# Kernel optimization log

Measured on AMD Instinct MI355X. Metric: run time of the kernel, lower is better.

## Reference

```python
import jax, jax.numpy as jnp
import numpy as np

HEADS = 8
EMBED = 512


def setup_inputs() -> dict:
    key = jax.random.key(0)
    ks = jax.random.split(key, 9)
    N, KL, QL, S = 4, 512, 32, 64
    D = EMBED // HEADS
    return {
        "values": jax.random.normal(ks[0], (N, KL, EMBED), jnp.float32),
        "keys": jax.random.normal(ks[1], (N, KL, EMBED), jnp.float32),
        "query": jax.random.normal(ks[2], (N, QL, S, EMBED), jnp.float32),
        "mask": jax.random.randint(ks[3], (N, 1, 1, KL, 1), 0, 2, jnp.int32),
        "Wv": jax.random.normal(ks[4], (D, D), jnp.float32) * 0.05,
        "Wk": jax.random.normal(ks[5], (D, D), jnp.float32) * 0.05,
        "Wq": jax.random.normal(ks[6], (D, D), jnp.float32) * 0.05,
        "Wo": jax.random.normal(ks[7], (EMBED, EMBED), jnp.float32) * 0.05,
        "bo": jax.random.normal(ks[8], (EMBED,), jnp.float32) * 0.05,
    }


def reference(values, keys, query, mask, Wv, Wk, Wq, Wo, bo):
    N, KL, E = keys.shape
    QL, S = query.shape[1], query.shape[2]
    H = HEADS
    D = E // H
    # split heads, then per-head linear (weights shared across heads, torch y = x @ W.T)
    v = jnp.einsum('nkhd,ed->nkhe', values.reshape(N, KL, H, D), Wv)
    k = jnp.einsum('nkhd,ed->nkhe', keys.reshape(N, KL, H, D), Wk)
    q = jnp.einsum('nqshd,ed->nqshe', query.reshape(N, QL, S, H, D), Wq)
    # energy: [N, H, QL, KL, S]
    energy = jnp.einsum('nqshd,nkhd->nhqks', q, k)
    energy = jnp.where(mask == 0, jnp.float32(-1e20), energy)
    scale = jnp.float32(E ** 0.5)
    attention = jax.nn.softmax(energy / scale, axis=3)  # softmax over key axis
    out = jnp.einsum('nhqks,nkhd->nqshd', attention, v).reshape(N, QL, S, E)
    return out @ Wo.T + bo
```

## Files before the change

kernel.cpp:

```cpp
#include <hip/hip_runtime.h>
#include <math.h>


typedef __bf16 bf16;
typedef __attribute__((ext_vector_type(8))) __bf16 bf16x8;
typedef __attribute__((ext_vector_type(4))) __bf16 bf16x4;
typedef __attribute__((ext_vector_type(4))) float f32x4;

#define LW 68
#define LS 72
#define QSCALE (0.044194173824159216f * 1.4426950408889634f)
#define MASK_BIAS -64.0f

__device__ __forceinline__ bf16x8 cvt8(const float* p, float s) {
    float4 x0 = *(const float4*)p;
    float4 x1 = *(const float4*)(p + 4);
    return (bf16x8){(bf16)(x0.x * s), (bf16)(x0.y * s), (bf16)(x0.z * s), (bf16)(x0.w * s),
                    (bf16)(x1.x * s), (bf16)(x1.y * s), (bf16)(x1.z * s), (bf16)(x1.w * s)};
}

__global__ __launch_bounds__(256, 2) void kv_proj(const float* __restrict__ keys,
                                                  const float* __restrict__ values,
                                                  const float* __restrict__ Wk,
                                                  const float* __restrict__ Wv,
                                                  bf16* __restrict__ Kp,
                                                  bf16* __restrict__ Vt) {
    __shared__ bf16 Xk[64 * LW];
    __shared__ bf16 Xv[64 * LW];
    int t = threadIdx.x;
    int nh = blockIdx.x >> 3, kt = blockIdx.x & 7;
    int n = nh >> 3, h = nh & 7, kl0 = kt * 64;
    int w = t >> 6, quad = (t >> 4) & 3, c16 = t & 15;
#pragma unroll
    for (int i = 0; i < 4; ++i) {
        int f = t + i * 256, row = f >> 4, c4 = f & 15;
        float4 a = *(const float4*)(keys + ((long)n * 512 + kl0 + row) * 512 + h * 64 + c4 * 4);
        float4 b = *(const float4*)(values + ((long)n * 512 + kl0 + row) * 512 + h * 64 + c4 * 4);
        *(bf16x4*)&Xk[row * LW + c4 * 4] = (bf16x4){(bf16)a.x, (bf16)a.y, (bf16)a.z, (bf16)a.w};
        *(bf16x4*)&Xv[row * LW + c4 * 4] = (bf16x4){(bf16)b.x, (bf16)b.y, (bf16)b.z, (bf16)b.w};
    }
    __syncthreads();
    if (w < 2) {
        bf16x8 wf[8];
#pragma unroll
        for (int nb = 0; nb < 4; ++nb)
#pragma unroll
            for (int kc = 0; kc < 2; ++kc)
                wf[nb * 2 + kc] = cvt8(Wk + (16 * nb + c16) * 64 + 32 * kc + quad * 8, 1.0f);
        f32x4 acc[2][4];
#pragma unroll
        for (int mb = 0; mb < 2; ++mb)
#pragma unroll
            for (int nb = 0; nb < 4; ++nb) acc[mb][nb] = (f32x4){0.f, 0.f, 0.f, 0.f};
#pragma unroll
        for (int kc = 0; kc < 2; ++kc) {
            bf16x8 a0 = *(const bf16x8*)&Xk[(32 * w + c16) * LW + 32 * kc + quad * 8];
            bf16x8 a1 = *(const bf16x8*)&Xk[(32 * w + 16 + c16) * LW + 32 * kc + quad * 8];
#pragma unroll
            for (int nb = 0; nb < 4; ++nb) {
                acc[0][nb] = __builtin_amdgcn_mfma_f32_16x16x32_bf16(a0, wf[nb * 2 + kc], acc[0][nb], 0, 0, 0);
                acc[1][nb] = __builtin_amdgcn_mfma_f32_16x16x32_bf16(a1, wf[nb * 2 + kc], acc[1][nb], 0, 0, 0);
            }
        }
#pragma unroll
        for (int mb = 0; mb < 2; ++mb)
#pragma unroll
            for (int nb = 0; nb < 4; ++nb)
#pragma unroll
                for (int r = 0; r < 4; ++r)
                    Kp[((long)nh * 512 + kl0 + 32 * w + 16 * mb + quad * 4 + r) * 64 + 16 * nb + c16] =
                        (bf16)acc[mb][nb][r];
    } else {
        int w2 = w - 2;
        bf16x8 af[4];
#pragma unroll
        for (int mb = 0; mb < 2; ++mb)
#pragma unroll
            for (int kc = 0; kc < 2; ++kc)
                af[mb * 2 + kc] = cvt8(Wv + (32 * w2 + 16 * mb + c16) * 64 + 32 * kc + quad * 8, 1.0f);
        f32x4 acc[2][4];
#pragma unroll
        for (int mb = 0; mb < 2; ++mb)
#pragma unroll
            for (int nb = 0; nb < 4; ++nb) acc[mb][nb] = (f32x4){0.f, 0.f, 0.f, 0.f};
#pragma unroll
        for (int kc = 0; kc < 2; ++kc) {
#pragma unroll
            for (int nb = 0; nb < 4; ++nb) {
                bf16x8 b = *(const bf16x8*)&Xv[(16 * nb + c16) * LW + 32 * kc + quad * 8];
                acc[0][nb] = __builtin_amdgcn_mfma_f32_16x16x32_bf16(af[kc], b, acc[0][nb], 0, 0, 0);
                acc[1][nb] = __builtin_amdgcn_mfma_f32_16x16x32_bf16(af[2 + kc], b, acc[1][nb], 0, 0, 0);
            }
        }
#pragma unroll
        for (int mb = 0; mb < 2; ++mb)
#pragma unroll
            for (int nb = 0; nb < 4; ++nb)
#pragma unroll
                for (int r = 0; r < 4; ++r)
                    Vt[((long)nh * 64 + 32 * w2 + 16 * mb + quad * 4 + r) * 512 + kl0 + 16 * nb + c16] =
                        (bf16)acc[mb][nb][r];
    }
}

__global__ __launch_bounds__(256, 4) void attn(const float* __restrict__ query,
                                               const float* __restrict__ Wq,
                                               const bf16* __restrict__ Kp,
                                               const bf16* __restrict__ Vtg,
                                               const int* __restrict__ maskp,
                                               bf16* __restrict__ AO) {
    __shared__ bf16 SX[64 * LS];
    __shared__ bf16 Kt[64 * LW];
    __shared__ bf16 Vs[64 * LW];
    __shared__ float Mb[64];
    int t = threadIdx.x;
    int nh = blockIdx.x & 31, qtile = blockIdx.x >> 5;
    int n = nh >> 3, h = nh & 7;
    int r0 = qtile * 64;
    int w = t >> 6, quad = (t >> 4) & 3, c16 = t & 15;
    const bf16* Kb = Kp + (long)nh * 512 * 64;
    const bf16* Vb = Vtg + (long)nh * 64 * 512;

    int prow0 = t >> 3, pcol0 = t & 7;
    int prow1 = (t + 256) >> 3, pcol1 = t & 7;
    bf16x8 pk0 = *(const bf16x8*)(Kb + (long)prow0 * 64 + pcol0 * 8);
    bf16x8 pk1 = *(const bf16x8*)(Kb + (long)prow1 * 64 + pcol1 * 8);
    bf16x8 pv0 = *(const bf16x8*)(Vb + (long)prow0 * 512 + pcol0 * 8);
    bf16x8 pv1 = *(const bf16x8*)(Vb + (long)prow1 * 512 + pcol1 * 8);
    float mnext = 0.f;
    if (t < 64) mnext = maskp[n * 512 + t] ? 0.f : MASK_BIAS;

    bf16x8 wf[8];
#pragma unroll
    for (int nb = 0; nb < 4; ++nb)
#pragma unroll
        for (int kc = 0; kc < 2; ++kc)
            wf[nb * 2 + kc] = cvt8(Wq + (16 * nb + c16) * 64 + 32 * kc + quad * 8, QSCALE);

    {
        int l = t & 63;
        int rloc = 16 * w + (l >> 2);
        const float* qrow = query + ((long)n * 2048 + r0 + rloc) * 512 + h * 64;
#pragma unroll
        for (int j = 0; j < 4; ++j) {
            int c = (l & 3) + 4 * j;
            float4 a = *(const float4*)(qrow + c * 4);
            *(bf16x4*)&SX[rloc * LS + c * 4] = (bf16x4){(bf16)a.x, (bf16)a.y, (bf16)a.z, (bf16)a.w};
        }
    }
    f32x4 qa[4];
#pragma unroll
    for (int nb = 0; nb < 4; ++nb) qa[nb] = (f32x4){0.f, 0.f, 0.f, 0.f};
#pragma unroll
    for (int kc = 0; kc < 2; ++kc) {
        bf16x8 a = *(const bf16x8*)&SX[(16 * w + c16) * LS + 32 * kc + quad * 8];
#pragma unroll
        for (int nb = 0; nb < 4; ++nb)
            qa[nb] = __builtin_amdgcn_mfma_f32_16x16x32_bf16(a, wf[nb * 2 + kc], qa[nb], 0, 0, 0);
    }
#pragma unroll
    for (int nb = 0; nb < 4; ++nb)
#pragma unroll
        for (int r = 0; r < 4; ++r)
            SX[(16 * w + quad * 4 + r) * LS + 16 * nb + c16] = (bf16)qa[nb][r];
    bf16x8 qf[2];
#pragma unroll
    for (int kc = 0; kc < 2; ++kc)
        qf[kc] = *(const bf16x8*)&SX[(16 * w + c16) * LS + 32 * kc + quad * 8];

    f32x4 oacc[4];
#pragma unroll
    for (int mb = 0; mb < 4; ++mb) oacc[mb] = (f32x4){0.f, 0.f, 0.f, 0.f};
    float ps = 0.f;

    for (int kt = 0; kt < 8; ++kt) {
        if (kt) __syncthreads();
        *(bf16x8*)&Kt[prow0 * LW + pcol0 * 8] = pk0;
        *(bf16x8*)&Kt[prow1 * LW + pcol1 * 8] = pk1;
        *(bf16x8*)&Vs[prow0 * LW + pcol0 * 8] = pv0;
        *(bf16x8*)&Vs[prow1 * LW + pcol1 * 8] = pv1;
        if (t < 64) Mb[t] = mnext;
        __syncthreads();
        if (kt < 7) {
            const bf16* Kn = Kb + (long)(kt + 1) * 64 * 64;
            const bf16* Vn = Vb + (kt + 1) * 64;
            pk0 = *(const bf16x8*)(Kn + (long)prow0 * 64 + pcol0 * 8);
            pk1 = *(const bf16x8*)(Kn + (long)prow1 * 64 + pcol1 * 8);
            pv0 = *(const bf16x8*)(Vn + (long)prow0 * 512 + pcol0 * 8);
            pv1 = *(const bf16x8*)(Vn + (long)prow1 * 512 + pcol1 * 8);
            if (t < 64) mnext = maskp[n * 512 + (kt + 1) * 64 + t] ? 0.f : MASK_BIAS;
        }
        f32x4 sc[4];
#pragma unroll
        for (int mb = 0; mb < 4; ++mb) sc[mb] = *(const f32x4*)&Mb[16 * mb + quad * 4];
#pragma unroll
        for (int kc = 0; kc < 2; ++kc) {
#pragma unroll
            for (int mb = 0; mb < 4; ++mb) {
                bf16x8 ka = *(const bf16x8*)&Kt[(16 * mb + c16) * LW + 32 * kc + quad * 8];
                sc[mb] = __builtin_amdgcn_mfma_f32_16x16x32_bf16(ka, qf[kc], sc[mb], 0, 0, 0);
            }
        }
#pragma unroll
        for (int mb = 0; mb < 4; ++mb) {
            float p0 = exp2f(sc[mb][0]);
            float p1 = exp2f(sc[mb][1]);
            float p2 = exp2f(sc[mb][2]);
            float p3 = exp2f(sc[mb][3]);
            ps += (p0 + p1) + (p2 + p3);
            *(bf16x4*)&SX[(16 * w + c16) * LS + 16 * mb + quad * 4] =
                (bf16x4){(bf16)p0, (bf16)p1, (bf16)p2, (bf16)p3};
        }
#pragma unroll
        for (int kc = 0; kc < 2; ++kc) {
            bf16x8 pb = *(const bf16x8*)&SX[(16 * w + c16) * LS + 32 * kc + quad * 8];
#pragma unroll
            for (int mb = 0; mb < 4; ++mb) {
                bf16x8 va = *(const bf16x8*)&Vs[(16 * mb + c16) * LW + 32 * kc + quad * 8];
                oacc[mb] = __builtin_amdgcn_mfma_f32_16x16x32_bf16(va, pb, oacc[mb], 0, 0, 0);
            }
        }
    }
    ps += __shfl_xor(ps, 16);
    ps += __shfl_xor(ps, 32);
    float il = 1.0f / ps;
    int row_g = r0 + 16 * w + c16;
#pragma unroll
    for (int mb = 0; mb < 4; ++mb)
        *(bf16x4*)(AO + ((long)n * 2048 + row_g) * 512 + h * 64 + 16 * mb + quad * 4) =
            (bf16x4){(bf16)(oacc[mb][0] * il), (bf16)(oacc[mb][1] * il),
                     (bf16)(oacc[mb][2] * il), (bf16)(oacc[mb][3] * il)};
}

__global__ __launch_bounds__(256, 2) void out_gemm(const bf16* __restrict__ A,
                                                   const float* __restrict__ Wo,
                                                   const float* __restrict__ bo,
                                                   float* __restrict__ C) {
    __shared__ bf16 At[128 * LW];
    __shared__ bf16 Bt[64 * LW];
    int t = threadIdx.x;
    int br = blockIdx.x & 63, bc = blockIdx.x >> 6;
    int r0 = br * 128, c0 = bc * 64;
    int w = t >> 6, quad = (t >> 4) & 3, c16 = t & 15;
    int arow[4], acol[4], wrow[4], wcol[4];
#pragma unroll
    for (int i = 0; i < 4; ++i) {
        int f = t + i * 256;
        arow[i] = f >> 3;
        acol[i] = f & 7;
        wrow[i] = f >> 4;
        wcol[i] = f & 15;
    }
    bf16x8 pa[4];
    float4 pw[4];
#pragma unroll
    for (int i = 0; i < 4; ++i) {
        pa[i] = *(const bf16x8*)(A + (long)(r0 + arow[i]) * 512 + acol[i] * 8);
        pw[i] = *(const float4*)(Wo + (long)(c0 + wrow[i]) * 512 + wcol[i] * 4);
    }
    f32x4 acc[2][4];
#pragma unroll
    for (int mb = 0; mb < 2; ++mb)
#pragma unroll
        for (int nb = 0; nb < 4; ++nb) acc[mb][nb] = (f32x4){0.f, 0.f, 0.f, 0.f};
    for (int k0 = 0; k0 < 512; k0 += 64) {
        if (k0) __syncthreads();
#pragma unroll
        for (int i = 0; i < 4; ++i) {
            *(bf16x8*)&At[arow[i] * LW + acol[i] * 8] = pa[i];
            *(bf16x4*)&Bt[wrow[i] * LW + wcol[i] * 4] =
                (bf16x4){(bf16)pw[i].x, (bf16)pw[i].y, (bf16)pw[i].z, (bf16)pw[i].w};
        }
        __syncthreads();
        if (k0 < 448) {
#pragma unroll
            for (int i = 0; i < 4; ++i) {
                pa[i] = *(const bf16x8*)(A + (long)(r0 + arow[i]) * 512 + k0 + 64 + acol[i] * 8);
                pw[i] = *(const float4*)(Wo + (long)(c0 + wrow[i]) * 512 + k0 + 64 + wcol[i] * 4);
            }
        }
#pragma unroll
        for (int kc = 0; kc < 2; ++kc) {
            bf16x8 a0 = *(const bf16x8*)&At[(32 * w + c16) * LW + 32 * kc + quad * 8];
            bf16x8 a1 = *(const bf16x8*)&At[(32 * w + 16 + c16) * LW + 32 * kc + quad * 8];
#pragma unroll
            for (int nb = 0; nb < 4; ++nb) {
                bf16x8 b = *(const bf16x8*)&Bt[(16 * nb + c16) * LW + 32 * kc + quad * 8];
                acc[0][nb] = __builtin_amdgcn_mfma_f32_16x16x32_bf16(a0, b, acc[0][nb], 0, 0, 0);
                acc[1][nb] = __builtin_amdgcn_mfma_f32_16x16x32_bf16(a1, b, acc[1][nb], 0, 0, 0);
            }
        }
    }
#pragma unroll
    for (int mb = 0; mb < 2; ++mb)
#pragma unroll
        for (int nb = 0; nb < 4; ++nb) {
            float bias = bo[c0 + 16 * nb + c16];
#pragma unroll
            for (int r = 0; r < 4; ++r)
                C[(long)(r0 + 32 * w + 16 * mb + quad * 4 + r) * 512 + c0 + 16 * nb + c16] =
                    acc[mb][nb][r] + bias;
        }
}

extern "C" void kernel_launch(void* const* d_in, const int* in_sizes, int n_in,
                              void* d_out, int out_size, void* d_ws, size_t ws_size,
                              hipStream_t stream) {
    const float* values = (const float*)d_in[0];
    const float* keys   = (const float*)d_in[1];
    const float* query  = (const float*)d_in[2];
    const int*   maskp  = (const int*)d_in[3];
    const float* Wv     = (const float*)d_in[4];
    const float* Wk     = (const float*)d_in[5];
    const float* Wq     = (const float*)d_in[6];
    const float* Wo     = (const float*)d_in[7];
    const float* bo     = (const float*)d_in[8];
    float* out = (float*)d_out;

    bf16* ws = (bf16*)d_ws;
    bf16* Kp = ws;
    bf16* Vt = Kp + 1048576;
    bf16* AO = Vt + 1048576;

    kv_proj<<<dim3(256), dim3(256), 0, stream>>>(keys, values, Wk, Wv, Kp, Vt);
    attn<<<dim3(1024), dim3(256), 0, stream>>>(query, Wq, Kp, Vt, maskp, AO);
    out_gemm<<<dim3(512), dim3(256), 0, stream>>>(AO, Wo, bo, out);
}
```

Before: 129.0 us.

## Split attention over key halves and merge partials in output GEMM

The attention kernel splits the key range into two halves per query tile, doubling the grid. Each half writes unnormalized bf16 partial outputs and row sums, and the output GEMM sums the two partials and normalizes while loading its A tile. The KV projection and output GEMM tiles are shrunk to launch more blocks, and the mask is read directly from global memory instead of staged in shared memory. This trades extra Q projection work and doubled intermediate traffic for higher occupancy and parallelism.

```diff
diff --git a/kernel.cpp b/kernel.cpp
--- a/kernel.cpp
+++ b/kernel.cpp
@@ -25,14 +25,14 @@
                                                   const float* __restrict__ Wv,
                                                   bf16* __restrict__ Kp,
                                                   bf16* __restrict__ Vt) {
-    __shared__ bf16 Xk[64 * LW];
-    __shared__ bf16 Xv[64 * LW];
+    __shared__ bf16 Xk[32 * LW];
+    __shared__ bf16 Xv[32 * LW];
     int t = threadIdx.x;
-    int nh = blockIdx.x >> 3, kt = blockIdx.x & 7;
-    int n = nh >> 3, h = nh & 7, kl0 = kt * 64;
+    int nh = blockIdx.x >> 4, klt = blockIdx.x & 15;
+    int n = nh >> 3, h = nh & 7, kl0 = klt * 32;
     int w = t >> 6, quad = (t >> 4) & 3, c16 = t & 15;
 #pragma unroll
-    for (int i = 0; i < 4; ++i) {
+    for (int i = 0; i < 2; ++i) {
         int f = t + i * 256, row = f >> 4, c4 = f & 15;
         float4 a = *(const float4*)(keys + ((long)n * 512 + kl0 + row) * 512 + h * 64 + c4 * 4);
         float4 b = *(const float4*)(values + ((long)n * 512 + kl0 + row) * 512 + h * 64 + c4 * 4);
@@ -41,61 +41,47 @@
     }
     __syncthreads();
     if (w < 2) {
-        bf16x8 wf[8];
+        f32x4 acc[4];
+#pragma unroll
+        for (int nb = 0; nb < 4; ++nb) acc[nb] = (f32x4){0.f, 0.f, 0.f, 0.f};
+#pragma unroll
+        for (int kc = 0; kc < 2; ++kc) {
+            bf16x8 a = *(const bf16x8*)&Xk[(16 * w + c16) * LW + 32 * kc + quad * 8];
+#pragma unroll
+            for (int nb = 0; nb < 4; ++nb) {
+                bf16x8 b = cvt8(Wk + (16 * nb + c16) * 64 + 32 * kc + quad * 8, 1.0f);
+                acc[nb] = __builtin_amdgcn_mfma_f32_16x16x32_bf16(a, b, acc[nb], 0, 0, 0);
+            }
+        }
 #pragma unroll
         for (int nb = 0; nb < 4; ++nb)
 #pragma unroll
-            for (int kc = 0; kc < 2; ++kc)
-                wf[nb * 2 + kc] = cvt8(Wk + (16 * nb + c16) * 64 + 32 * kc + quad * 8, 1.0f);
-        f32x4 acc[2][4];
-#pragma unroll
-        for (int mb = 0; mb < 2; ++mb)
-#pragma unroll
-            for (int nb = 0; nb < 4; ++nb) acc[mb][nb] = (f32x4){0.f, 0.f, 0.f, 0.f};
-#pragma unroll
-        for (int kc = 0; kc < 2; ++kc) {
-            bf16x8 a0 = *(const bf16x8*)&Xk[(32 * w + c16) * LW + 32 * kc + quad * 8];
-            bf16x8 a1 = *(const bf16x8*)&Xk[(32 * w + 16 + c16) * LW + 32 * kc + quad * 8];
-#pragma unroll
-            for (int nb = 0; nb < 4; ++nb) {
-                acc[0][nb] = __builtin_amdgcn_mfma_f32_16x16x32_bf16(a0, wf[nb * 2 + kc], acc[0][nb], 0, 0, 0);
-                acc[1][nb] = __builtin_amdgcn_mfma_f32_16x16x32_bf16(a1, wf[nb * 2 + kc], acc[1][nb], 0, 0, 0);
-            }
-        }
-#pragma unroll
-        for (int mb = 0; mb < 2; ++mb)
-#pragma unroll
-            for (int nb = 0; nb < 4; ++nb)
-#pragma unroll
-                for (int r = 0; r < 4; ++r)
-                    Kp[((long)nh * 512 + kl0 + 32 * w + 16 * mb + quad * 4 + r) * 64 + 16 * nb + c16] =
-                        (bf16)acc[mb][nb][r];
+            for (int r = 0; r < 4; ++r)
+                Kp[((long)nh * 512 + kl0 + 16 * w + quad * 4 + r) * 64 + 16 * nb + c16] =
+                    (bf16)acc[nb][r];
     } else {
         int w2 = w - 2;
-        bf16x8 af[4];
+        f32x4 acc[2][2];
 #pragma unroll
         for (int mb = 0; mb < 2; ++mb)
 #pragma unroll
-            for (int kc = 0; kc < 2; ++kc)
-                af[mb * 2 + kc] = cvt8(Wv + (32 * w2 + 16 * mb + c16) * 64 + 32 * kc + quad * 8, 1.0f);
-        f32x4 acc[2][4];
+            for (int nb = 0; nb < 2; ++nb) acc[mb][nb] = (f32x4){0.f, 0.f, 0.f, 0.f};
+#pragma unroll
+        for (int kc = 0; kc < 2; ++kc) {
+#pragma unroll
+            for (int mb = 0; mb < 2; ++mb) {
+                bf16x8 a = cvt8(Wv + (32 * w2 + 16 * mb + c16) * 64 + 32 * kc + quad * 8, 1.0f);
+#pragma unroll
+                for (int nb = 0; nb < 2; ++nb) {
+                    bf16x8 b = *(const bf16x8*)&Xv[(16 * nb + c16) * LW + 32 * kc + quad * 8];
+                    acc[mb][nb] = __builtin_amdgcn_mfma_f32_16x16x32_bf16(a, b, acc[mb][nb], 0, 0, 0);
+                }
+            }
+        }
 #pragma unroll
         for (int mb = 0; mb < 2; ++mb)
 #pragma unroll
-            for (int nb = 0; nb < 4; ++nb) acc[mb][nb] = (f32x4){0.f, 0.f, 0.f, 0.f};
-#pragma unroll
-        for (int kc = 0; kc < 2; ++kc) {
-#pragma unroll
-            for (int nb = 0; nb < 4; ++nb) {
-                bf16x8 b = *(const bf16x8*)&Xv[(16 * nb + c16) * LW + 32 * kc + quad * 8];
-                acc[0][nb] = __builtin_amdgcn_mfma_f32_16x16x32_bf16(af[kc], b, acc[0][nb], 0, 0, 0);
-                acc[1][nb] = __builtin_amdgcn_mfma_f32_16x16x32_bf16(af[2 + kc], b, acc[1][nb], 0, 0, 0);
-            }
-        }
-#pragma unroll
-        for (int mb = 0; mb < 2; ++mb)
-#pragma unroll
-            for (int nb = 0; nb < 4; ++nb)
+            for (int nb = 0; nb < 2; ++nb)
 #pragma unroll
                 for (int r = 0; r < 4; ++r)
                     Vt[((long)nh * 64 + 32 * w2 + 16 * mb + quad * 4 + r) * 512 + kl0 + 16 * nb + c16] =
@@ -108,27 +94,26 @@
                                                const bf16* __restrict__ Kp,
                                                const bf16* __restrict__ Vtg,
                                                const int* __restrict__ maskp,
-                                               bf16* __restrict__ AO) {
+                                               bf16* __restrict__ AOp,
+                                               float* __restrict__ Lb) {
     __shared__ bf16 SX[64 * LS];
     __shared__ bf16 Kt[64 * LW];
     __shared__ bf16 Vs[64 * LW];
-    __shared__ float Mb[64];
     int t = threadIdx.x;
-    int nh = blockIdx.x & 31, qtile = blockIdx.x >> 5;
+    int nh = blockIdx.x & 31, half = (blockIdx.x >> 5) & 1, qtile = blockIdx.x >> 6;
     int n = nh >> 3, h = nh & 7;
     int r0 = qtile * 64;
+    int kt0 = half * 4;
     int w = t >> 6, quad = (t >> 4) & 3, c16 = t & 15;
     const bf16* Kb = Kp + (long)nh * 512 * 64;
     const bf16* Vb = Vtg + (long)nh * 64 * 512;
 
     int prow0 = t >> 3, pcol0 = t & 7;
     int prow1 = (t + 256) >> 3, pcol1 = t & 7;
-    bf16x8 pk0 = *(const bf16x8*)(Kb + (long)prow0 * 64 + pcol0 * 8);
-    bf16x8 pk1 = *(const bf16x8*)(Kb + (long)prow1 * 64 + pcol1 * 8);
-    bf16x8 pv0 = *(const bf16x8*)(Vb + (long)prow0 * 512 + pcol0 * 8);
-    bf16x8 pv1 = *(const bf16x8*)(Vb + (long)prow1 * 512 + pcol1 * 8);
-    float mnext = 0.f;
-    if (t < 64) mnext = maskp[n * 512 + t] ? 0.f : MASK_BIAS;
+    bf16x8 pk0 = *(const bf16x8*)(Kb + (long)(kt0 * 64 + prow0) * 64 + pcol0 * 8);
+    bf16x8 pk1 = *(const bf16x8*)(Kb + (long)(kt0 * 64 + prow1) * 64 + pcol1 * 8);
+    bf16x8 pv0 = *(const bf16x8*)(Vb + (long)prow0 * 512 + kt0 * 64 + pcol0 * 8);
+    bf16x8 pv1 = *(const bf16x8*)(Vb + (long)prow1 * 512 + kt0 * 64 + pcol1 * 8);
 
     bf16x8 wf[8];
 #pragma unroll
@@ -173,26 +158,27 @@
     for (int mb = 0; mb < 4; ++mb) oacc[mb] = (f32x4){0.f, 0.f, 0.f, 0.f};
     float ps = 0.f;
 
-    for (int kt = 0; kt < 8; ++kt) {
+    for (int kt = 0; kt < 4; ++kt) {
+        int tk = kt0 + kt;
         if (kt) __syncthreads();
         *(bf16x8*)&Kt[prow0 * LW + pcol0 * 8] = pk0;
         *(bf16x8*)&Kt[prow1 * LW + pcol1 * 8] = pk1;
         *(bf16x8*)&Vs[prow0 * LW + pcol0 * 8] = pv0;
         *(bf16x8*)&Vs[prow1 * LW + pcol1 * 8] = pv1;
-        if (t < 64) Mb[t] = mnext;
         __syncthreads();
-        if (kt < 7) {
-            const bf16* Kn = Kb + (long)(kt + 1) * 64 * 64;
-            const bf16* Vn = Vb + (kt + 1) * 64;
-            pk0 = *(const bf16x8*)(Kn + (long)prow0 * 64 + pcol0 * 8);
-            pk1 = *(const bf16x8*)(Kn + (long)prow1 * 64 + pcol1 * 8);
-            pv0 = *(const bf16x8*)(Vn + (long)prow0 * 512 + pcol0 * 8);
-            pv1 = *(const bf16x8*)(Vn + (long)prow1 * 512 + pcol1 * 8);
-            if (t < 64) mnext = maskp[n * 512 + (kt + 1) * 64 + t] ? 0.f : MASK_BIAS;
+        if (kt < 3) {
+            pk0 = *(const bf16x8*)(Kb + (long)((tk + 1) * 64 + prow0) * 64 + pcol0 * 8);
+            pk1 = *(const bf16x8*)(Kb + (long)((tk + 1) * 64 + prow1) * 64 + pcol1 * 8);
+            pv0 = *(const bf16x8*)(Vb + (long)prow0 * 512 + (tk + 1) * 64 + pcol0 * 8);
+            pv1 = *(const bf16x8*)(Vb + (long)prow1 * 512 + (tk + 1) * 64 + pcol1 * 8);
         }
         f32x4 sc[4];
 #pragma unroll
-        for (int mb = 0; mb < 4; ++mb) sc[mb] = *(const f32x4*)&Mb[16 * mb + quad * 4];
+        for (int mb = 0; mb < 4; ++mb) {
+            int4 mk = *(const int4*)(maskp + n * 512 + tk * 64 + 16 * mb + quad * 4);
+            sc[mb] = (f32x4){mk.x ? 0.f : MASK_BIAS, mk.y ? 0.f : MASK_BIAS,
+                             mk.z ? 0.f : MASK_BIAS, mk.w ? 0.f : MASK_BIAS};
+        }
 #pragma unroll
         for (int kc = 0; kc < 2; ++kc) {
 #pragma unroll
@@ -223,84 +209,99 @@
     }
     ps += __shfl_xor(ps, 16);
     ps += __shfl_xor(ps, 32);
-    float il = 1.0f / ps;
     int row_g = r0 + 16 * w + c16;
+    bf16* AO = AOp + (long)half * 4194304;
 #pragma unroll
     for (int mb = 0; mb < 4; ++mb)
         *(bf16x4*)(AO + ((long)n * 2048 + row_g) * 512 + h * 64 + 16 * mb + quad * 4) =
-            (bf16x4){(bf16)(oacc[mb][0] * il), (bf16)(oacc[mb][1] * il),
-                     (bf16)(oacc[mb][2] * il), (bf16)(oacc[mb][3] * il)};
-}
-
-__global__ __launch_bounds__(256, 2) void out_gemm(const bf16* __restrict__ A,
+            (bf16x4){(bf16)oacc[mb][0], (bf16)oacc[mb][1], (bf16)oacc[mb][2], (bf16)oacc[mb][3]};
+    if (quad == 0) Lb[half * 65536 + nh * 2048 + row_g] = ps;
+}
+
+__global__ __launch_bounds__(256, 4) void out_gemm(const bf16* __restrict__ AOp,
+                                                   const float* __restrict__ Lb,
                                                    const float* __restrict__ Wo,
                                                    const float* __restrict__ bo,
                                                    float* __restrict__ C) {
-    __shared__ bf16 At[128 * LW];
+    __shared__ bf16 At[64 * LW];
     __shared__ bf16 Bt[64 * LW];
     int t = threadIdx.x;
-    int br = blockIdx.x & 63, bc = blockIdx.x >> 6;
-    int r0 = br * 128, c0 = bc * 64;
+    int br = blockIdx.x & 127, bc = blockIdx.x >> 7;
+    int r0 = br * 64, c0 = bc * 64;
     int w = t >> 6, quad = (t >> 4) & 3, c16 = t & 15;
-    int arow[4], acol[4], wrow[4], wcol[4];
-#pragma unroll
-    for (int i = 0; i < 4; ++i) {
+    const bf16* AO2 = AOp + 4194304;
+    int arow[2], acol[2], wrow[4], wcol[4];
+#pragma unroll
+    for (int i = 0; i < 2; ++i) {
         int f = t + i * 256;
         arow[i] = f >> 3;
         acol[i] = f & 7;
+    }
+#pragma unroll
+    for (int i = 0; i < 4; ++i) {
+        int f = t + i * 256;
         wrow[i] = f >> 4;
         wcol[i] = f & 15;
     }
-    bf16x8 pa[4];
+    bf16x8 pa1[2], pa2[2];
     float4 pw[4];
 #pragma unroll
-    for (int i = 0; i < 4; ++i) {
-        pa[i] = *(const bf16x8*)(A + (long)(r0 + arow[i]) * 512 + acol[i] * 8);
+    for (int i = 0; i < 2; ++i) {
+        pa1[i] = *(const bf16x8*)(AOp + (long)(r0 + arow[i]) * 512 + acol[i] * 8);
+        pa2[i] = *(const bf16x8*)(AO2 + (long)(r0 + arow[i]) * 512 + acol[i] * 8);
+    }
+#pragma unroll
+    for (int i = 0; i < 4; ++i)
         pw[i] = *(const float4*)(Wo + (long)(c0 + wrow[i]) * 512 + wcol[i] * 4);
-    }
-    f32x4 acc[2][4];
-#pragma unroll
-    for (int mb = 0; mb < 2; ++mb)
-#pragma unroll
-        for (int nb = 0; nb < 4; ++nb) acc[mb][nb] = (f32x4){0.f, 0.f, 0.f, 0.f};
+    f32x4 acc[4];
+#pragma unroll
+    for (int nb = 0; nb < 4; ++nb) acc[nb] = (f32x4){0.f, 0.f, 0.f, 0.f};
     for (int k0 = 0; k0 < 512; k0 += 64) {
+        int hh = k0 >> 6;
         if (k0) __syncthreads();
 #pragma unroll
-        for (int i = 0; i < 4; ++i) {
-            *(bf16x8*)&At[arow[i] * LW + acol[i] * 8] = pa[i];
+        for (int i = 0; i < 2; ++i) {
+            int grow = r0 + arow[i];
+            int lidx = ((grow >> 11) * 8 + hh) * 2048 + (grow & 2047);
+            float il = 1.0f / (Lb[lidx] + Lb[65536 + lidx]);
+            bf16x8 o;
+#pragma unroll
+            for (int e = 0; e < 8; ++e)
+                o[e] = (bf16)(((float)pa1[i][e] + (float)pa2[i][e]) * il);
+            *(bf16x8*)&At[arow[i] * LW + acol[i] * 8] = o;
+        }
+#pragma unroll
+        for (int i = 0; i < 4; ++i)
             *(bf16x4*)&Bt[wrow[i] * LW + wcol[i] * 4] =
                 (bf16x4){(bf16)pw[i].x, (bf16)pw[i].y, (bf16)pw[i].z, (bf16)pw[i].w};
-        }
         __syncthreads();
         if (k0 < 448) {
 #pragma unroll
-            for (int i = 0; i < 4; ++i) {
-                pa[i] = *(const bf16x8*)(A + (long)(r0 + arow[i]) * 512 + k0 + 64 + acol[i] * 8);
+            for (int i = 0; i < 2; ++i) {
+                pa1[i] = *(const bf16x8*)(AOp + (long)(r0 + arow[i]) * 512 + k0 + 64 + acol[i] * 8);
+                pa2[i] = *(const bf16x8*)(AO2 + (long)(r0 + arow[i]) * 512 + k0 + 64 + acol[i] * 8);
+            }
+#pragma unroll
+            for (int i = 0; i < 4; ++i)
                 pw[i] = *(const float4*)(Wo + (long)(c0 + wrow[i]) * 512 + k0 + 64 + wcol[i] * 4);
-            }
-        }
-#pragma unroll
-        for (int kc = 0; kc < 2; ++kc) {
-            bf16x8 a0 = *(const bf16x8*)&At[(32 * w + c16) * LW + 32 * kc + quad * 8];
-            bf16x8 a1 = *(const bf16x8*)&At[(32 * w + 16 + c16) * LW + 32 * kc + quad * 8];
+        }
+#pragma unroll
+        for (int kc = 0; kc < 2; ++kc) {
+            bf16x8 a = *(const bf16x8*)&At[(16 * w + c16) * LW + 32 * kc + quad * 8];
 #pragma unroll
             for (int nb = 0; nb < 4; ++nb) {
                 bf16x8 b = *(const bf16x8*)&Bt[(16 * nb + c16) * LW + 32 * kc + quad * 8];
-                acc[0][nb] = __builtin_amdgcn_mfma_f32_16x16x32_bf16(a0, b, acc[0][nb], 0, 0, 0);
-                acc[1][nb] = __builtin_amdgcn_mfma_f32_16x16x32_bf16(a1, b, acc[1][nb], 0, 0, 0);
-            }
-        }
-    }
-#pragma unroll
-    for (int mb = 0; mb < 2; ++mb)
-#pragma unroll
-        for (int nb = 0; nb < 4; ++nb) {
-            float bias = bo[c0 + 16 * nb + c16];
-#pragma unroll
-            for (int r = 0; r < 4; ++r)
-                C[(long)(r0 + 32 * w + 16 * mb + quad * 4 + r) * 512 + c0 + 16 * nb + c16] =
-                    acc[mb][nb][r] + bias;
-        }
+                acc[nb] = __builtin_amdgcn_mfma_f32_16x16x32_bf16(a, b, acc[nb], 0, 0, 0);
+            }
+        }
+    }
+#pragma unroll
+    for (int nb = 0; nb < 4; ++nb) {
+        float bias = bo[c0 + 16 * nb + c16];
+#pragma unroll
+        for (int r = 0; r < 4; ++r)
+            C[(long)(r0 + 16 * w + quad * 4 + r) * 512 + c0 + 16 * nb + c16] = acc[nb][r] + bias;
+    }
 }
 
 extern "C" void kernel_launch(void* const* d_in, const int* in_sizes, int n_in,
@@ -318,11 +319,12 @@
     float* out = (float*)d_out;
 
     bf16* ws = (bf16*)d_ws;
-    bf16* Kp = ws;
-    bf16* Vt = Kp + 1048576;
-    bf16* AO = Vt + 1048576;
-
-    kv_proj<<<dim3(256), dim3(256), 0, stream>>>(keys, values, Wk, Wv, Kp, Vt);
-    attn<<<dim3(1024), dim3(256), 0, stream>>>(query, Wq, Kp, Vt, maskp, AO);
-    out_gemm<<<dim3(512), dim3(256), 0, stream>>>(AO, Wo, bo, out);
-}
+    bf16* Kp  = ws;
+    bf16* Vt  = Kp + 1048576;
+    bf16* AOp = Vt + 1048576;
+    float* Lb = (float*)(AOp + 8388608);
+
+    kv_proj<<<dim3(512), dim3(256), 0, stream>>>(keys, values, Wk, Wv, Kp, Vt);
+    attn<<<dim3(2048), dim3(256), 0, stream>>>(query, Wq, Kp, Vt, maskp, AOp, Lb);
+    out_gemm<<<dim3(1024), dim3(256), 0, stream>>>(AOp, Lb, Wo, bo, out);
+}
```

New measurement: 144.2 us. 1.12x slower.
